# Kernel optimization log

Hardware: AMD Instinct MI355X
Metric: run time of the kernel (lower is better)

## Reference

```python
import jax, jax.numpy as jnp
import numpy as np

KERNEL = 7
STRIDE = 3
C_IN, C_OUT = 3, 4
HIDDEN, OUTPUT = 64, 10
H_OUT = (32 - KERNEL) // STRIDE + 1  # 9
FC1_IN = C_OUT * H_OUT * H_OUT       # 324


def setup_inputs() -> dict:
    key = jax.random.key(0)
    ks = jax.random.split(key, 6)
    B = 16384
    x = jax.random.normal(ks[0], (B, C_IN, 32, 32), dtype=jnp.float32)
    conv_w = jax.random.normal(ks[1], (C_OUT, C_IN, KERNEL, KERNEL), dtype=jnp.float32) * 0.05
    fc1_w = jax.random.normal(ks[2], (HIDDEN, FC1_IN), dtype=jnp.float32) * (1.0 / np.sqrt(FC1_IN))
    fc1_b = jax.random.normal(ks[3], (HIDDEN,), dtype=jnp.float32) * 0.01
    fc2_w = jax.random.normal(ks[4], (OUTPUT, HIDDEN), dtype=jnp.float32) * (1.0 / np.sqrt(HIDDEN))
    fc2_b = jax.random.normal(ks[5], (OUTPUT,), dtype=jnp.float32) * 0.01
    return {"x": x, "conv_w": conv_w, "fc1_w": fc1_w, "fc1_b": fc1_b, "fc2_w": fc2_w, "fc2_b": fc2_b}


def reference(x, conv_w, fc1_w, fc1_b, fc2_w, fc2_b):
    # conv (NO bias, matching original forward which only uses conv1.weight)
    y = jax.lax.conv_general_dilated(
        x, conv_w, window_strides=(STRIDE, STRIDE), padding='VALID',
        dimension_numbers=('NCHW', 'OIHW', 'NCHW'))  # [B, 4, 9, 9]
    y = y * y
    y = y.reshape(y.shape[0], -1)                    # [B, 324]
    h = y @ fc1_w.T + fc1_b                          # [B, 64]
    h = h * h
    out = h @ fc2_w.T + fc2_b                        # [B, 10]
    return out
```

## Files before the change

kernel.cpp:

```cpp
#include <hip/hip_runtime.h>
#include <string.h>


typedef _Float16 f16;
typedef f16 f16x8 __attribute__((ext_vector_type(8)));
typedef __fp16 fp16x2 __attribute__((ext_vector_type(2)));
typedef float f32x4 __attribute__((ext_vector_type(4)));

#define YS_B   13824
#define LDS_B  (13824 + 11520)

__device__ __forceinline__ unsigned pack_rtz(float a, float b) {
    fp16x2 h = __builtin_amdgcn_cvt_pkrtz(a, b);
    unsigned u; memcpy(&u, &h, 4); return u;
}

__device__ __forceinline__ void write_half(f16* wptr, const float4 ldv[5], int half) {
    unsigned h[10];
#pragma unroll
    for (int i = 0; i < 5; ++i) {
        h[2*i]   = pack_rtz(ldv[i].x, ldv[i].y);
        h[2*i+1] = pack_rtz(ldv[i].z, ldv[i].w);
    }
    const int owb = half * 4;
    if (!half) {
        uint4 v; v.x = h[0]; v.y = h[1]; v.z = h[2]; v.w = h[3];
        *reinterpret_cast<uint4*>(wptr) = v;
    }
    {
        uint4 v;
        v.x = __builtin_amdgcn_alignbit(h[2], h[1], 16);
        v.y = __builtin_amdgcn_alignbit(h[3], h[2], 16);
        v.z = __builtin_amdgcn_alignbit(h[4], h[3], 16);
        v.w = __builtin_amdgcn_alignbit(h[5], h[4], 16);
        *reinterpret_cast<uint4*>(wptr + (owb + 1) * 8) = v;
    }
    {
        uint4 v; v.x = h[3]; v.y = h[4]; v.z = h[5]; v.w = h[6];
        *reinterpret_cast<uint4*>(wptr + (owb + 2) * 8) = v;
    }
    {
        uint4 v;
        v.x = __builtin_amdgcn_alignbit(h[5], h[4], 16);
        v.y = __builtin_amdgcn_alignbit(h[6], h[5], 16);
        v.z = __builtin_amdgcn_alignbit(h[7], h[6], 16);
        v.w = __builtin_amdgcn_alignbit(h[8], h[7], 16);
        *reinterpret_cast<uint4*>(wptr + (owb + 3) * 8) = v;
    }
    {
        uint4 v; v.x = h[6]; v.y = h[7]; v.z = h[8]; v.w = h[9];
        *reinterpret_cast<uint4*>(wptr + (owb + 4) * 8) = v;
    }
}

__global__ __launch_bounds__(256, 6) void convnet_mfma(
    const float* __restrict__ x,
    const float* __restrict__ cw,
    const float* __restrict__ fc1w,
    const float* __restrict__ fc1b,
    const float* __restrict__ fc2w,
    const float* __restrict__ fc2b,
    float* __restrict__ out)
{
    __shared__ unsigned char lds[LDS_B];
    f16* WINH = (f16*)lds;
    f16* YS   = (f16*)(lds + YS_B);
    float* HSQ = (float*)lds;

    const int t    = threadIdx.x;
    const int lane = t & 63;
    const int w    = t >> 6;
    const int g    = lane >> 4;
    const int lr   = lane & 15;
    const size_t base_s = (size_t)blockIdx.x * 16;

    f16x8 wcf[6];
#pragma unroll
    for (int st = 0; st < 6; ++st) {
        f16x8 v = {0, 0, 0, 0, 0, 0, 0, 0};
        int seg = st * 4 + g;
        if (lr < 4 && seg <= 20) {
            int ci = seg >= 14 ? 2 : (seg >= 7 ? 1 : 0);
            int kh = seg - ci * 7;
            const float* wr = cw + ((lr * 3 + ci) * 7 + kh) * 7;
#pragma unroll
            for (int j = 0; j < 7; ++j) v[j] = (f16)wr[j];
        }
        wcf[st] = v;
    }

    int seg2off[6];
#pragma unroll
    for (int st = 0; st < 6; ++st) {
        int seg  = st * 4 + g;
        int segc = seg > 20 ? 20 : seg;
        int ci   = segc >= 14 ? 2 : (segc >= 7 ? 1 : 0);
        int kh   = segc - ci * 7;
        seg2off[st] = ci * 4608 + kh * 144;
    }

    const int u = 3 - w;
    const int ntiles = (u < 2) ? 2 : 1;
    int rowbase[2], pbase[2];
#pragma unroll
    for (int ti = 0; ti < 2; ++ti) {
        int tile = u + ti * 4;
        int tc   = tile > 5 ? 5 : tile;
        int grow = tc * 16 + lr;
        int p    = grow > 80 ? 80 : grow;
        int oh   = (p * 57) >> 9;
        int ow   = p - oh * 9;
        rowbase[ti] = oh * 432 + ow * 16;
        pbase[ti]   = tc * 16 + g * 4;
    }

    const bool stg  = t < 192;
    const int  r_   = t >> 1;
    const int  half = t & 1;
    const int  sci  = r_ >> 5;
    const int  srow = r_ & 31;
    const int  goff = sci * 1024 + srow * 32 + (half ? 12 : 0);
    f16* wptr = WINH + sci * 2304 + srow * 72;

    float4 ldv[5];
    if (stg) {
        const float* gp = x + base_s * 3072 + goff;
#pragma unroll
        for (int i = 0; i < 5; ++i) ldv[i] = *(const float4*)(gp + 4 * i);
    }
#pragma unroll
    for (int i = 0; i < 3; ++i) {
        int idx = i * 256 + t;
        if (idx < 720) *(f32x4*)(lds + YS_B + idx * 16) = f32x4{0.f, 0.f, 0.f, 0.f};
    }
    if (stg) write_half(wptr, ldv, half);
    __syncthreads();

    for (int s = 0; s < 16; ++s) {
        if (s < 15 && stg) {
            const float* gp = x + (base_s + s + 1) * 3072 + goff;
#pragma unroll
            for (int i = 0; i < 5; ++i) ldv[i] = *(const float4*)(gp + 4 * i);
        }
        f16* ysp = YS + s * 360;
        __builtin_amdgcn_s_setprio(1);
#pragma unroll
        for (int ti = 0; ti < 2; ++ti) {
            if (ti < ntiles) {
                const unsigned char* pA = lds + rowbase[ti];
                f32x4 acc = {0.f, 0.f, 0.f, 0.f};
#pragma unroll
                for (int st = 0; st < 6; ++st) {
                    f16x8 af = *(const f16x8*)(pA + seg2off[st]);
                    acc = __builtin_amdgcn_mfma_f32_16x16x32_f16(af, wcf[st], acc, 0, 0, 0);
                }
                if (lr < 4) {
#pragma unroll
                    for (int r = 0; r < 4; ++r) {
                        int p = pbase[ti] + r;
                        if (p < 81) {
                            float y = acc[r];
                            ysp[lr * 81 + p] = (f16)(y * y);
                        }
                    }
                }
            }
        }
        __builtin_amdgcn_s_setprio(0);
        __syncthreads();
        if (s < 15) {
            if (stg) write_half(wptr, ldv, half);
            __syncthreads();
        }
    }

    {
        f32x4 a1 = {0.f, 0.f, 0.f, 0.f};
        const int n = w * 16 + lr;
        const float* w1r = fc1w + n * 324;
        __builtin_amdgcn_s_setprio(1);
#pragma unroll
        for (int st = 0; st < 10; ++st) {
            f16x8 av = *(const f16x8*)(YS + lr * 360 + st * 32 + g * 8);
            float4 v0 = *(const float4*)(w1r + st * 32 + g * 8);
            float4 v1 = *(const float4*)(w1r + st * 32 + g * 8 + 4);
            float vv[8] = {v0.x, v0.y, v0.z, v0.w, v1.x, v1.y, v1.z, v1.w};
            f16x8 bh, bl;
#pragma unroll
            for (int j = 0; j < 8; ++j) {
                f16 hi = (f16)vv[j];
                bh[j] = hi;
                bl[j] = (f16)(vv[j] - (float)hi);
            }
            a1 = __builtin_amdgcn_mfma_f32_16x16x32_f16(av, bh, a1, 0, 0, 0);
            a1 = __builtin_amdgcn_mfma_f32_16x16x32_f16(av, bl, a1, 0, 0, 0);
        }
        {
            f16x8 av = *(const f16x8*)(YS + lr * 360 + 320 + g * 8);
            f16x8 bh = {0,0,0,0,0,0,0,0}, bl = {0,0,0,0,0,0,0,0};
            if (g == 0) {
                float4 v0 = *(const float4*)(w1r + 320);
                float vv[4] = {v0.x, v0.y, v0.z, v0.w};
#pragma unroll
                for (int j = 0; j < 4; ++j) {
                    f16 hi = (f16)vv[j];
                    bh[j] = hi;
                    bl[j] = (f16)(vv[j] - (float)hi);
                }
            }
            a1 = __builtin_amdgcn_mfma_f32_16x16x32_f16(av, bh, a1, 0, 0, 0);
            a1 = __builtin_amdgcn_mfma_f32_16x16x32_f16(av, bl, a1, 0, 0, 0);
        }
        __builtin_amdgcn_s_setprio(0);
        float bias = fc1b[n];
#pragma unroll
        for (int r = 0; r < 4; ++r) {
            int s = g * 4 + r;
            float h = a1[r] + bias;
            HSQ[s * 65 + n] = h * h;
        }
    }
    __syncthreads();

    if (t < 160) {
        int sj = t / 10, j = t - sj * 10;
        float a = fc2b[j];
        const float* wr = fc2w + j * 64;
        const float* hv = &HSQ[sj * 65];
#pragma unroll
        for (int i = 0; i < 64; ++i) a += wr[i] * hv[i];
        out[(base_s + sj) * 10 + j] = a;
    }
}

extern "C" void kernel_launch(void* const* d_in, const int* in_sizes, int n_in,
                              void* d_out, int out_size, void* d_ws, size_t ws_size,
                              hipStream_t stream) {
    const float* x    = (const float*)d_in[0];
    const float* cw   = (const float*)d_in[1];
    const float* fc1w = (const float*)d_in[2];
    const float* fc1b = (const float*)d_in[3];
    const float* fc2w = (const float*)d_in[4];
    const float* fc2b = (const float*)d_in[5];
    float* out = (float*)d_out;

    const int B = in_sizes[0] / 3072;
    hipLaunchKernelGGL(convnet_mfma, dim3(B / 16), dim3(256), 0, stream,
                       x, cw, fc1w, fc1b, fc2w, fc2b, out);
}
```

Baseline: 45.50 us.

## Precompute fp16 weight splits in prep kernel and halve samples per block

Adds a prep kernel that converts the conv weights and the fc1 weights (split into hi and lo fp16 parts, padded to 352) into workspace once per call. The main kernel then loads ready fp16 fragments instead of converting from fp32 in every block. Samples per block drop from 16 to 8, which doubles the grid and shrinks LDS, and launch bounds go from 6 to 5. The cost is that the fc1 MFMA now runs at half utilisation, since rows 8-15 duplicate rows 0-7, and there is an extra kernel launch.

```diff
diff --git a/kernel.cpp b/kernel.cpp
--- a/kernel.cpp
+++ b/kernel.cpp
@@ -7,8 +7,9 @@
 typedef __fp16 fp16x2 __attribute__((ext_vector_type(2)));
 typedef float f32x4 __attribute__((ext_vector_type(4)));
 
+#define NS     8
 #define YS_B   13824
-#define LDS_B  (13824 + 11520)
+#define LDS_B  (13824 + NS * 720)
 
 __device__ __forceinline__ unsigned pack_rtz(float a, float b) {
     fp16x2 h = __builtin_amdgcn_cvt_pkrtz(a, b);
@@ -53,10 +54,33 @@
     }
 }
 
-__global__ __launch_bounds__(256, 6) void convnet_mfma(
+__global__ void prep_weights(const float* __restrict__ cw, const float* __restrict__ fc1w,
+                             f16* __restrict__ w1t, f16* __restrict__ wct) {
+    int idx = blockIdx.x * 256 + threadIdx.x;
+    if (idx < 45056) {
+        int part = idx / 22528;
+        int rem  = idx % 22528;
+        int n = rem / 352, k = rem % 352;
+        float v = (k < 324) ? fc1w[n * 324 + k] : 0.f;
+        f16 hi = (f16)v;
+        w1t[idx] = (part == 0) ? hi : (f16)(v - (float)hi);
+    } else {
+        int j = idx - 45056;
+        int oc = j / 192, k = j % 192;
+        int seg = k >> 3, kw = k & 7;
+        float v = 0.f;
+        if (oc < 4 && seg < 21 && kw < 7) {
+            int ci = seg / 7, kh = seg % 7;
+            v = cw[((oc * 3 + ci) * 7 + kh) * 7 + kw];
+        }
+        wct[j] = (f16)v;
+    }
+}
+
+__global__ __launch_bounds__(256, 5) void convnet_mfma(
     const float* __restrict__ x,
-    const float* __restrict__ cw,
-    const float* __restrict__ fc1w,
+    const f16*  __restrict__ w1t,
+    const f16*  __restrict__ wct,
     const float* __restrict__ fc1b,
     const float* __restrict__ fc2w,
     const float* __restrict__ fc2b,
@@ -72,22 +96,12 @@
     const int w    = t >> 6;
     const int g    = lane >> 4;
     const int lr   = lane & 15;
-    const size_t base_s = (size_t)blockIdx.x * 16;
+    const size_t base_s = (size_t)blockIdx.x * NS;
 
     f16x8 wcf[6];
 #pragma unroll
-    for (int st = 0; st < 6; ++st) {
-        f16x8 v = {0, 0, 0, 0, 0, 0, 0, 0};
-        int seg = st * 4 + g;
-        if (lr < 4 && seg <= 20) {
-            int ci = seg >= 14 ? 2 : (seg >= 7 ? 1 : 0);
-            int kh = seg - ci * 7;
-            const float* wr = cw + ((lr * 3 + ci) * 7 + kh) * 7;
-#pragma unroll
-            for (int j = 0; j < 7; ++j) v[j] = (f16)wr[j];
-        }
-        wcf[st] = v;
-    }
+    for (int st = 0; st < 6; ++st)
+        wcf[st] = *(const f16x8*)(wct + lr * 192 + st * 32 + g * 8);
 
     int seg2off[6];
 #pragma unroll
@@ -128,16 +142,15 @@
 #pragma unroll
         for (int i = 0; i < 5; ++i) ldv[i] = *(const float4*)(gp + 4 * i);
     }
-#pragma unroll
-    for (int i = 0; i < 3; ++i) {
-        int idx = i * 256 + t;
-        if (idx < 720) *(f32x4*)(lds + YS_B + idx * 16) = f32x4{0.f, 0.f, 0.f, 0.f};
+    if (t < NS * 18) {
+        int si = t / 18, d = t % 18;
+        *(unsigned*)(YS + si * 360 + 324 + d * 2) = 0u;
     }
     if (stg) write_half(wptr, ldv, half);
     __syncthreads();
 
-    for (int s = 0; s < 16; ++s) {
-        if (s < 15 && stg) {
+    for (int s = 0; s < NS; ++s) {
+        if (s < NS - 1 && stg) {
             const float* gp = x + (base_s + s + 1) * 3072 + goff;
 #pragma unroll
             for (int i = 0; i < 5; ++i) ldv[i] = *(const float4*)(gp + 4 * i);
@@ -168,7 +181,7 @@
         }
         __builtin_amdgcn_s_setprio(0);
         __syncthreads();
-        if (s < 15) {
+        if (s < NS - 1) {
             if (stg) write_half(wptr, ldv, half);
             __syncthreads();
         }
@@ -177,52 +190,29 @@
     {
         f32x4 a1 = {0.f, 0.f, 0.f, 0.f};
         const int n = w * 16 + lr;
-        const float* w1r = fc1w + n * 324;
         __builtin_amdgcn_s_setprio(1);
 #pragma unroll
-        for (int st = 0; st < 10; ++st) {
-            f16x8 av = *(const f16x8*)(YS + lr * 360 + st * 32 + g * 8);
-            float4 v0 = *(const float4*)(w1r + st * 32 + g * 8);
-            float4 v1 = *(const float4*)(w1r + st * 32 + g * 8 + 4);
-            float vv[8] = {v0.x, v0.y, v0.z, v0.w, v1.x, v1.y, v1.z, v1.w};
-            f16x8 bh, bl;
-#pragma unroll
-            for (int j = 0; j < 8; ++j) {
-                f16 hi = (f16)vv[j];
-                bh[j] = hi;
-                bl[j] = (f16)(vv[j] - (float)hi);
-            }
+        for (int st = 0; st < 11; ++st) {
+            f16x8 av = *(const f16x8*)(YS + (lr & 7) * 360 + st * 32 + g * 8);
+            f16x8 bh = *(const f16x8*)(w1t +          n * 352 + st * 32 + g * 8);
+            f16x8 bl = *(const f16x8*)(w1t + 22528 +  n * 352 + st * 32 + g * 8);
             a1 = __builtin_amdgcn_mfma_f32_16x16x32_f16(av, bh, a1, 0, 0, 0);
             a1 = __builtin_amdgcn_mfma_f32_16x16x32_f16(av, bl, a1, 0, 0, 0);
         }
-        {
-            f16x8 av = *(const f16x8*)(YS + lr * 360 + 320 + g * 8);
-            f16x8 bh = {0,0,0,0,0,0,0,0}, bl = {0,0,0,0,0,0,0,0};
-            if (g == 0) {
-                float4 v0 = *(const float4*)(w1r + 320);
-                float vv[4] = {v0.x, v0.y, v0.z, v0.w};
-#pragma unroll
-                for (int j = 0; j < 4; ++j) {
-                    f16 hi = (f16)vv[j];
-                    bh[j] = hi;
-                    bl[j] = (f16)(vv[j] - (float)hi);
-                }
-            }
-            a1 = __builtin_amdgcn_mfma_f32_16x16x32_f16(av, bh, a1, 0, 0, 0);
-            a1 = __builtin_amdgcn_mfma_f32_16x16x32_f16(av, bl, a1, 0, 0, 0);
-        }
         __builtin_amdgcn_s_setprio(0);
         float bias = fc1b[n];
 #pragma unroll
         for (int r = 0; r < 4; ++r) {
             int s = g * 4 + r;
-            float h = a1[r] + bias;
-            HSQ[s * 65 + n] = h * h;
+            if (s < NS) {
+                float h = a1[r] + bias;
+                HSQ[s * 65 + n] = h * h;
+            }
         }
     }
     __syncthreads();
 
-    if (t < 160) {
+    if (t < NS * 10) {
         int sj = t / 10, j = t - sj * 10;
         float a = fc2b[j];
         const float* wr = fc2w + j * 64;
@@ -244,7 +234,12 @@
     const float* fc2b = (const float*)d_in[5];
     float* out = (float*)d_out;
 
+    f16* w1t = (f16*)d_ws;
+    f16* wct = w1t + 45056;
+
+    hipLaunchKernelGGL(prep_weights, dim3(188), dim3(256), 0, stream, cw, fc1w, w1t, wct);
+
     const int B = in_sizes[0] / 3072;
-    hipLaunchKernelGGL(convnet_mfma, dim3(B / 16), dim3(256), 0, stream,
-                       x, cw, fc1w, fc1b, fc2w, fc2b, out);
-}
+    hipLaunchKernelGGL(convnet_mfma, dim3(B / NS), dim3(256), 0, stream,
+                       x, w1t, wct, fc1b, fc2w, fc2b, out);
+}
```

Result: slower. 57.86 us (+27.2%).

## Double-buffer conv input windows and overlap staging with MFMA compute

Applied to the files above, without the earlier changes.

Adds a second LDS window buffer so that the next sample's windows are written while the current one is consumed, dropping one barrier per sample. The global load now runs two samples ahead. Staging moves from 192 threads loading half-rows to 96 threads loading full rows, and tile assignment across waves is rebalanced. Only the YS padding is zeroed now, not the whole buffer. LDS use grows and launch bounds drop from 6 to 4 blocks per CU, which may reduce occupancy.

```diff
diff --git a/kernel.cpp b/kernel.cpp
--- a/kernel.cpp
+++ b/kernel.cpp
@@ -7,53 +7,35 @@
 typedef __fp16 fp16x2 __attribute__((ext_vector_type(2)));
 typedef float f32x4 __attribute__((ext_vector_type(4)));
 
-#define YS_B   13824
-#define LDS_B  (13824 + 11520)
+#define WIN_B  13824
+#define YS_B   27648
+#define LDS_B  (27648 + 11520)
 
 __device__ __forceinline__ unsigned pack_rtz(float a, float b) {
     fp16x2 h = __builtin_amdgcn_cvt_pkrtz(a, b);
     unsigned u; memcpy(&u, &h, 4); return u;
 }
 
-__device__ __forceinline__ void write_half(f16* wptr, const float4 ldv[5], int half) {
-    unsigned h[10];
-#pragma unroll
-    for (int i = 0; i < 5; ++i) {
-        h[2*i]   = pack_rtz(ldv[i].x, ldv[i].y);
-        h[2*i+1] = pack_rtz(ldv[i].z, ldv[i].w);
-    }
-    const int owb = half * 4;
-    if (!half) {
-        uint4 v; v.x = h[0]; v.y = h[1]; v.z = h[2]; v.w = h[3];
-        *reinterpret_cast<uint4*>(wptr) = v;
-    }
-    {
+__device__ __forceinline__ void write_windows(f16* wptr, const unsigned h[16]) {
+#pragma unroll
+    for (int ow = 0; ow < 9; ow += 2) {
+        int d = (3 * ow) >> 1;
+        uint4 v; v.x = h[d]; v.y = h[d+1]; v.z = h[d+2]; v.w = h[d+3];
+        *reinterpret_cast<uint4*>(wptr + ow * 8) = v;
+    }
+#pragma unroll
+    for (int ow = 1; ow < 9; ow += 2) {
+        int d = (3 * ow) >> 1;
         uint4 v;
-        v.x = __builtin_amdgcn_alignbit(h[2], h[1], 16);
-        v.y = __builtin_amdgcn_alignbit(h[3], h[2], 16);
-        v.z = __builtin_amdgcn_alignbit(h[4], h[3], 16);
-        v.w = __builtin_amdgcn_alignbit(h[5], h[4], 16);
-        *reinterpret_cast<uint4*>(wptr + (owb + 1) * 8) = v;
-    }
-    {
-        uint4 v; v.x = h[3]; v.y = h[4]; v.z = h[5]; v.w = h[6];
-        *reinterpret_cast<uint4*>(wptr + (owb + 2) * 8) = v;
-    }
-    {
-        uint4 v;
-        v.x = __builtin_amdgcn_alignbit(h[5], h[4], 16);
-        v.y = __builtin_amdgcn_alignbit(h[6], h[5], 16);
-        v.z = __builtin_amdgcn_alignbit(h[7], h[6], 16);
-        v.w = __builtin_amdgcn_alignbit(h[8], h[7], 16);
-        *reinterpret_cast<uint4*>(wptr + (owb + 3) * 8) = v;
-    }
-    {
-        uint4 v; v.x = h[6]; v.y = h[7]; v.z = h[8]; v.w = h[9];
-        *reinterpret_cast<uint4*>(wptr + (owb + 4) * 8) = v;
-    }
-}
-
-__global__ __launch_bounds__(256, 6) void convnet_mfma(
+        v.x = __builtin_amdgcn_alignbit(h[d+1], h[d],   16);
+        v.y = __builtin_amdgcn_alignbit(h[d+2], h[d+1], 16);
+        v.z = __builtin_amdgcn_alignbit(h[d+3], h[d+2], 16);
+        v.w = __builtin_amdgcn_alignbit(h[d+4], h[d+3], 16);
+        *reinterpret_cast<uint4*>(wptr + ow * 8) = v;
+    }
+}
+
+__global__ __launch_bounds__(256, 4) void convnet_mfma(
     const float* __restrict__ x,
     const float* __restrict__ cw,
     const float* __restrict__ fc1w,
@@ -63,7 +45,6 @@
     float* __restrict__ out)
 {
     __shared__ unsigned char lds[LDS_B];
-    f16* WINH = (f16*)lds;
     f16* YS   = (f16*)(lds + YS_B);
     float* HSQ = (float*)lds;
 
@@ -99,13 +80,13 @@
         seg2off[st] = ci * 4608 + kh * 144;
     }
 
-    const int u = 3 - w;
-    const int ntiles = (u < 2) ? 2 : 1;
+    const int ntiles = (w >= 2) ? 2 : 1;
+    const int tileA  = (w == 0) ? 2 : (w == 1) ? 5 : (w == 2) ? 0 : 1;
+    const int tileB  = (w == 2) ? 3 : 4;
     int rowbase[2], pbase[2];
 #pragma unroll
     for (int ti = 0; ti < 2; ++ti) {
-        int tile = u + ti * 4;
-        int tc   = tile > 5 ? 5 : tile;
+        int tc   = ti ? tileB : tileA;
         int grow = tc * 16 + lr;
         int p    = grow > 80 ? 80 : grow;
         int oh   = (p * 57) >> 9;
@@ -114,40 +95,50 @@
         pbase[ti]   = tc * 16 + g * 4;
     }
 
-    const bool stg  = t < 192;
-    const int  r_   = t >> 1;
-    const int  half = t & 1;
-    const int  sci  = r_ >> 5;
-    const int  srow = r_ & 31;
-    const int  goff = sci * 1024 + srow * 32 + (half ? 12 : 0);
-    f16* wptr = WINH + sci * 2304 + srow * 72;
-
-    float4 ldv[5];
+    const bool stg  = t < 96;
+    const int  sci  = t >> 5;
+    const int  srow = t & 31;
+    const int  goff = sci * 1024 + srow * 32;
+    const int  woff = sci * 2304 + srow * 72;
+
+    float4 ldv[8];
+    unsigned hh[16];
     if (stg) {
         const float* gp = x + base_s * 3072 + goff;
 #pragma unroll
-        for (int i = 0; i < 5; ++i) ldv[i] = *(const float4*)(gp + 4 * i);
-    }
-#pragma unroll
-    for (int i = 0; i < 3; ++i) {
+        for (int i = 0; i < 8; ++i) ldv[i] = *(const float4*)(gp + 4 * i);
+    }
+#pragma unroll
+    for (int i = 0; i < 2; ++i) {
         int idx = i * 256 + t;
-        if (idx < 720) *(f32x4*)(lds + YS_B + idx * 16) = f32x4{0.f, 0.f, 0.f, 0.f};
-    }
-    if (stg) write_half(wptr, ldv, half);
+        if (idx < 288) {
+            int si = idx / 18, d = idx - si * 18;
+            *(unsigned*)(YS + si * 360 + 324 + d * 2) = 0u;
+        }
+    }
+    if (stg) {
+#pragma unroll
+        for (int i = 0; i < 8; ++i) {
+            hh[2*i]   = pack_rtz(ldv[i].x, ldv[i].y);
+            hh[2*i+1] = pack_rtz(ldv[i].z, ldv[i].w);
+        }
+        write_windows((f16*)(lds) + woff, hh);
+        const float* gp = x + (base_s + 1) * 3072 + goff;
+#pragma unroll
+        for (int i = 0; i < 8; ++i) ldv[i] = *(const float4*)(gp + 4 * i);
+    }
     __syncthreads();
 
     for (int s = 0; s < 16; ++s) {
-        if (s < 15 && stg) {
-            const float* gp = x + (base_s + s + 1) * 3072 + goff;
-#pragma unroll
-            for (int i = 0; i < 5; ++i) ldv[i] = *(const float4*)(gp + 4 * i);
-        }
-        f16* ysp = YS + s * 360;
+        const unsigned char* winb = lds + (s & 1) * WIN_B;
+        f16* wino = (f16*)(lds + ((s & 1) ^ 1) * WIN_B);
+        f16* ysp  = YS + s * 360;
+
         __builtin_amdgcn_s_setprio(1);
 #pragma unroll
         for (int ti = 0; ti < 2; ++ti) {
             if (ti < ntiles) {
-                const unsigned char* pA = lds + rowbase[ti];
+                const unsigned char* pA = winb + rowbase[ti];
                 f32x4 acc = {0.f, 0.f, 0.f, 0.f};
 #pragma unroll
                 for (int st = 0; st < 6; ++st) {
@@ -167,11 +158,21 @@
             }
         }
         __builtin_amdgcn_s_setprio(0);
+
+        if (s < 15 && stg) {
+#pragma unroll
+            for (int i = 0; i < 8; ++i) {
+                hh[2*i]   = pack_rtz(ldv[i].x, ldv[i].y);
+                hh[2*i+1] = pack_rtz(ldv[i].z, ldv[i].w);
+            }
+            write_windows(wino + woff, hh);
+        }
+        if (s < 14 && stg) {
+            const float* gp = x + (base_s + s + 2) * 3072 + goff;
+#pragma unroll
+            for (int i = 0; i < 8; ++i) ldv[i] = *(const float4*)(gp + 4 * i);
+        }
         __syncthreads();
-        if (s < 15) {
-            if (stg) write_half(wptr, ldv, half);
-            __syncthreads();
-        }
     }
 
     {
```

New measurement: 45.98 us. Within noise of the previous version (+1.0%).
